# Optimization experiments

Hardware: AMD Instinct MI355X
Metric: run time of the kernel (lower is better)

Reference implementation:

```python
import jax, jax.numpy as jnp
import numpy as np

B, C_IN, C_OUT, H, W = 4, 256, 256, 64, 64
KH = KW = 3
STRIDE = 1
PAD = 1
DIL = 1


def setup_inputs() -> dict:
    key = jax.random.key(0)
    k1, k2, k3, k4 = jax.random.split(key, 4)
    x = jax.random.normal(k1, (B, C_IN, H, W), dtype=jnp.float32)
    # torchvision layout: 2*dg*KH*KW channels, (y, x) pair per kernel tap
    offset = jax.random.normal(k2, (B, 2 * KH * KW, H, W), dtype=jnp.float32)
    fan_in = C_IN * KH * KW
    weight = jax.random.normal(k3, (C_OUT, C_IN, KH, KW), dtype=jnp.float32) / np.sqrt(fan_in)
    bias = jax.random.normal(k4, (C_OUT,), dtype=jnp.float32) * 0.01
    return {"x": x, "offset": offset, "weight": weight, "bias": bias}


def _gather_bilinear_corner(x_flat, yi, xi, h, w):
    # x_flat: [B, C, H*W]; yi/xi: [B, KK, Ho, Wo] int32
    valid = ((yi >= 0) & (yi < h) & (xi >= 0) & (xi < w)).astype(x_flat.dtype)
    idx = jnp.clip(yi, 0, h - 1) * w + jnp.clip(xi, 0, w - 1)
    b = idx.shape[0]
    g = jnp.take_along_axis(x_flat, idx.reshape(b, 1, -1), axis=2)
    return g.reshape(b, x_flat.shape[1], *yi.shape[1:]), valid


def deform_conv2d(x, offset, weight, bias):
    b, c, h, w = x.shape
    o = weight.shape[0]
    kk = KH * KW
    ho = (h + 2 * PAD - DIL * (KH - 1) - 1) // STRIDE + 1
    wo = (w + 2 * PAD - DIL * (KW - 1) - 1) // STRIDE + 1

    ky = (jnp.arange(kk, dtype=jnp.float32) // KW) * DIL  # [KK]
    kx = (jnp.arange(kk, dtype=jnp.float32) % KW) * DIL
    hs = jnp.arange(ho, dtype=jnp.float32) * STRIDE - PAD   # [Ho]
    ws = jnp.arange(wo, dtype=jnp.float32) * STRIDE - PAD   # [Wo]

    off = offset.reshape(b, kk, 2, ho, wo)
    py = hs[None, None, :, None] + ky[None, :, None, None] + off[:, :, 0]  # [B,KK,Ho,Wo]
    px = ws[None, None, None, :] + kx[None, :, None, None] + off[:, :, 1]

    y0 = jnp.floor(py)
    x0 = jnp.floor(px)
    wy1 = py - y0  # fractional parts, differentiable w.r.t. offsets
    wx1 = px - x0
    wy0 = 1.0 - wy1
    wx0 = 1.0 - wx1
    y0i = y0.astype(jnp.int32)
    x0i = x0.astype(jnp.int32)

    x_flat = x.reshape(b, c, h * w)
    corners = [
        (y0i,     x0i,     wy0 * wx0),
        (y0i,     x0i + 1, wy0 * wx1),
        (y0i + 1, x0i,     wy1 * wx0),
        (y0i + 1, x0i + 1, wy1 * wx1),
    ]
    sampled = jnp.zeros((b, c, kk, ho, wo), dtype=x.dtype)
    for yi, xi, wgt in corners:
        g, valid = _gather_bilinear_corner(x_flat, yi, xi, h, w)
        sampled = sampled + g * (wgt * valid)[:, None]

    out = jnp.einsum('bckhw,ock->bohw', sampled, weight.reshape(o, c, kk))
    return out + bias[None, :, None, None]


def reference(x, offset, weight, bias):
    return deform_conv2d(x, offset, weight, bias)
```

## Files before the change

kernel.cpp:

```cpp
#include <hip/hip_runtime.h>

typedef __bf16 bf16;
typedef __bf16 bf16x4 __attribute__((ext_vector_type(4)));
typedef __bf16 bf16x8 __attribute__((ext_vector_type(8)));
typedef float  f32x4  __attribute__((ext_vector_type(4)));

#define CIN   256
#define KK    9
#define KDIM  2304
#define KITERS 72
#define PXW   64

__device__ __forceinline__ float sread(float f) {
    return __builtin_bit_cast(float,
        __builtin_amdgcn_readfirstlane(__builtin_bit_cast(int, f)));
}
__device__ __forceinline__ int sreadi(int v) {
    return __builtin_amdgcn_readfirstlane(v);
}

__global__ __launch_bounds__(256) void prep_k(const float* __restrict__ x,
                                              const float* __restrict__ w,
                                              bf16* __restrict__ xt,
                                              bf16* __restrict__ wq) {
    int bid = blockIdx.x;
    int tid = threadIdx.x;
    if (bid < 1024) {
        __shared__ bf16 tile[64][72];
        int pt = bid & 63, ct = (bid >> 6) & 3, b = bid >> 8;
        int lane = tid & 63, row = tid >> 6;
        const float* src = x + ((size_t)(b * 256 + ct * 64)) * 4096 + pt * 64;
        #pragma unroll
        for (int cc = row; cc < 64; cc += 4)
            tile[lane][cc] = (bf16)src[(size_t)cc * 4096 + lane];
        __syncthreads();
        bf16* dst = xt + ((size_t)(b * 4096 + pt * 64)) * 256 + ct * 64;
        int p = tid >> 3, j = tid & 7;
        #pragma unroll
        for (int pp = p; pp < 64; pp += 32)
            *reinterpret_cast<bf16x8*>(dst + (size_t)pp * 256 + j * 8) =
                *reinterpret_cast<const bf16x8*>(&tile[pp][j * 8]);
    } else {
        int idx  = (bid - 1024) * 256 + tid;
        int j    = idx & 7;
        int lane = (idx >> 3) & 63;
        int rest = idx >> 9;
        int kt   = rest % KITERS;
        int m    = rest / KITERS;
        int l16  = lane & 15;
        int quad = lane >> 4;
        int o    = m * 16 + l16;
        int k    = kt * 32 + quad * 8 + j;
        int tap  = k >> 8;
        int cc   = k & 255;
        wq[idx] = (bf16)w[(size_t)o * KDIM + cc * KK + tap];
    }
}

__global__ __launch_bounds__(1024, 4) void deform_gemm_k(
    const bf16*  __restrict__ xt,
    const float* __restrict__ off,
    const bf16*  __restrict__ wq,
    const float* __restrict__ bias,
    float*       __restrict__ out) {

    __shared__ bf16 S[PXW * 256];

    int tid   = threadIdx.x;
    int wavei = sreadi(tid >> 6);
    int lane  = tid & 63;
    int quad  = lane >> 4;
    int l16   = lane & 15;

    int bid   = blockIdx.x;
    int pb    = ((bid & 7) << 5) | (bid >> 3);
    int pix0  = pb * PXW;
    int b     = pix0 >> 12;
    int pimgb = pix0 & 4095;
    int obase = b * 73728;
    unsigned base = (unsigned)b * 1048576u + (unsigned)(lane * 4);

    f32x4 acc[4];
    #pragma unroll
    for (int nt = 0; nt < 4; ++nt)
        acc[nt] = (f32x4){0.f, 0.f, 0.f, 0.f};

    int q3 = lane & 7;

    for (int tap = 0; tap < KK; ++tap) {
        int ty = tap / 3 - 1;
        int tx = tap % 3 - 1;

        int u[4][4];
        float wt[4][4];
        #pragma unroll
        for (int i = 0; i < 4; ++i) {
            int pimg = pimgb + wavei * 4 + i;
            float oy = off[obase + pimg + (2 * tap) * 4096];
            float ox = off[obase + pimg + (2 * tap + 1) * 4096];
            float py = (float)((pimg >> 6) + ty) + oy;
            float px = (float)((pimg & 63) + tx) + ox;
            float fy = floorf(py), fx = floorf(px);
            int   y0 = (int)fy,    x0 = (int)fx;
            float wy1 = py - fy, wx1 = px - fx;
            float wy0 = 1.f - wy1, wx0 = 1.f - wx1;
            wy0 = ((unsigned)y0       < 64u) ? wy0 : 0.f;
            wy1 = ((unsigned)(y0 + 1) < 64u) ? wy1 : 0.f;
            wx0 = ((unsigned)x0       < 64u) ? wx0 : 0.f;
            wx1 = ((unsigned)(x0 + 1) < 64u) ? wx1 : 0.f;
            int yc0 = min(max(y0, 0), 63),     yc1 = min(max(y0 + 1, 0), 63);
            int xc0 = min(max(x0, 0), 63),     xc1 = min(max(x0 + 1, 0), 63);
            u[i][0] = sreadi((yc0 * 64 + xc0) * 256);
            u[i][1] = sreadi((yc0 * 64 + xc1) * 256);
            u[i][2] = sreadi((yc1 * 64 + xc0) * 256);
            u[i][3] = sreadi((yc1 * 64 + xc1) * 256);
            wt[i][0] = sread(wy0 * wx0); wt[i][1] = sread(wy0 * wx1);
            wt[i][2] = sread(wy1 * wx0); wt[i][3] = sread(wy1 * wx1);
        }
        bf16x4 v[4][4];
        #pragma unroll
        for (int i = 0; i < 4; ++i)
            #pragma unroll
            for (int j = 0; j < 4; ++j)
                v[i][j] = *reinterpret_cast<const bf16x4*>(xt + base + (unsigned)u[i][j]);
        #pragma unroll
        for (int i = 0; i < 4; ++i) {
            float a0 = 0.f, a1 = 0.f, a2 = 0.f, a3 = 0.f;
            #pragma unroll
            for (int j = 0; j < 4; ++j) {
                float wgt = wt[i][j];
                a0 += wgt * (float)v[i][j][0];
                a1 += wgt * (float)v[i][j][1];
                a2 += wgt * (float)v[i][j][2];
                a3 += wgt * (float)v[i][j][3];
            }
            bf16x4 sv;
            sv[0] = (bf16)a0; sv[1] = (bf16)a1;
            sv[2] = (bf16)a2; sv[3] = (bf16)a3;
            int n   = wavei * 4 + i;
            int gsw = (lane >> 1) ^ (n & 7);
            *reinterpret_cast<bf16x4*>(&S[n * 256 + gsw * 8 + (lane & 1) * 4]) = sv;
        }
        __syncthreads();

        const bf16* ap0 = wq + ((size_t)((wavei * KITERS + tap * 8) * 64 + lane)) * 8;
        #pragma unroll
        for (int kki = 0; kki < 8; ++kki) {
            bf16x8 a = *reinterpret_cast<const bf16x8*>(ap0 + (size_t)kki * 512);
            #pragma unroll
            for (int nt = 0; nt < 4; ++nt) {
                int row = nt * 16 + l16;
                int g   = (kki * 4 + quad) ^ q3;
                bf16x8 bb = *reinterpret_cast<const bf16x8*>(&S[row * 256 + g * 8]);
                acc[nt] = __builtin_amdgcn_mfma_f32_16x16x32_bf16(a, bb, acc[nt], 0, 0, 0);
            }
        }
        __syncthreads();
    }

    #pragma unroll
    for (int nt = 0; nt < 4; ++nt) {
        int pg   = pix0 + nt * 16 + l16;
        int bb_  = pg >> 12;
        int pimg = pg & 4095;
        int m    = wavei * 16 + quad * 4;
        float* op = out + ((size_t)(bb_ * 256 + m)) * 4096 + pimg;
        #pragma unroll
        for (int r = 0; r < 4; ++r)
            op[(size_t)r * 4096] = acc[nt][r] + bias[m + r];
    }
}

extern "C" void kernel_launch(void* const* d_in, const int* in_sizes, int n_in,
                              void* d_out, int out_size, void* d_ws, size_t ws_size,
                              hipStream_t stream) {
    const float* x    = (const float*)d_in[0];
    const float* off  = (const float*)d_in[1];
    const float* w    = (const float*)d_in[2];
    const float* bias = (const float*)d_in[3];
    float* out = (float*)d_out;

    bf16* wq = (bf16*)d_ws;
    bf16* xt = (bf16*)((char*)d_ws + (size_t)589824 * 2);

    prep_k<<<3328, 256, 0, stream>>>(x, w, xt, wq);
    deform_gemm_k<<<256, 1024, 0, stream>>>(xt, off, wq, bias, out);
}
```

Baseline: 121.2 us.

## Warp-specialize deform conv into gather producers and MFMA consumers with slot ring

Splits the 16 waves into 8 producer waves that do the bilinear gather into a 3-slot LDS ring of half-tap chunks and 8 consumer waves that run the MFMAs. Each consumer wave now computes two output-row tiles. Producers and consumers coordinate through shared-memory ready/freed counters with spin-sleep instead of block-wide barriers. The aim is to overlap gather latency with matrix math. The cost is that only half the waves gather and half compute, consumers carry doubled accumulators, and busy-wait polling is added.

```diff
diff --git a/kernel.cpp b/kernel.cpp
--- a/kernel.cpp
+++ b/kernel.cpp
@@ -10,6 +10,8 @@
 #define KDIM  2304
 #define KITERS 72
 #define PXW   64
+#define NSLOT 3
+#define SLOT_ELEMS (PXW * 128)
 
 __device__ __forceinline__ float sread(float f) {
     return __builtin_bit_cast(float,
@@ -57,14 +59,16 @@
     }
 }
 
-__global__ __launch_bounds__(1024, 4) void deform_gemm_k(
+__global__ __launch_bounds__(1024) void deform_gemm_k(
     const bf16*  __restrict__ xt,
     const float* __restrict__ off,
     const bf16*  __restrict__ wq,
     const float* __restrict__ bias,
     float*       __restrict__ out) {
 
-    __shared__ bf16 S[PXW * 256];
+    __shared__ bf16 S[NSLOT * SLOT_ELEMS];
+    __shared__ int ready[NSLOT];
+    __shared__ int freed[NSLOT];
 
     int tid   = threadIdx.x;
     int wavei = sreadi(tid >> 6);
@@ -78,96 +82,133 @@
     int b     = pix0 >> 12;
     int pimgb = pix0 & 4095;
     int obase = b * 73728;
-    unsigned base = (unsigned)b * 1048576u + (unsigned)(lane * 4);
-
-    f32x4 acc[4];
-    #pragma unroll
-    for (int nt = 0; nt < 4; ++nt)
-        acc[nt] = (f32x4){0.f, 0.f, 0.f, 0.f};
-
-    int q3 = lane & 7;
-
-    for (int tap = 0; tap < KK; ++tap) {
-        int ty = tap / 3 - 1;
-        int tx = tap % 3 - 1;
-
-        int u[4][4];
-        float wt[4][4];
-        #pragma unroll
-        for (int i = 0; i < 4; ++i) {
-            int pimg = pimgb + wavei * 4 + i;
-            float oy = off[obase + pimg + (2 * tap) * 4096];
-            float ox = off[obase + pimg + (2 * tap + 1) * 4096];
-            float py = (float)((pimg >> 6) + ty) + oy;
-            float px = (float)((pimg & 63) + tx) + ox;
-            float fy = floorf(py), fx = floorf(px);
-            int   y0 = (int)fy,    x0 = (int)fx;
-            float wy1 = py - fy, wx1 = px - fx;
-            float wy0 = 1.f - wy1, wx0 = 1.f - wx1;
-            wy0 = ((unsigned)y0       < 64u) ? wy0 : 0.f;
-            wy1 = ((unsigned)(y0 + 1) < 64u) ? wy1 : 0.f;
-            wx0 = ((unsigned)x0       < 64u) ? wx0 : 0.f;
-            wx1 = ((unsigned)(x0 + 1) < 64u) ? wx1 : 0.f;
-            int yc0 = min(max(y0, 0), 63),     yc1 = min(max(y0 + 1, 0), 63);
-            int xc0 = min(max(x0, 0), 63),     xc1 = min(max(x0 + 1, 0), 63);
-            u[i][0] = sreadi((yc0 * 64 + xc0) * 256);
-            u[i][1] = sreadi((yc0 * 64 + xc1) * 256);
-            u[i][2] = sreadi((yc1 * 64 + xc0) * 256);
-            u[i][3] = sreadi((yc1 * 64 + xc1) * 256);
-            wt[i][0] = sread(wy0 * wx0); wt[i][1] = sread(wy0 * wx1);
-            wt[i][2] = sread(wy1 * wx0); wt[i][3] = sread(wy1 * wx1);
+
+    if (tid < NSLOT) { ready[tid] = 0; freed[tid] = 0; }
+    __syncthreads();
+
+    if (wavei < 8) {
+        int pw = wavei;
+        unsigned base = (unsigned)b * 1048576u + (unsigned)(lane * 4);
+        for (int tap = 0; tap < KK; ++tap) {
+            int ty = tap / 3 - 1;
+            int tx = tap % 3 - 1;
+            int h0 = 2 * tap,     s0 = h0 % 3, g0 = h0 / 3;
+            int h1 = 2 * tap + 1, s1 = h1 % 3, g1 = h1 / 3;
+            while (*(volatile int*)&freed[s0] < 8 * g0) __builtin_amdgcn_s_sleep(2);
+            while (*(volatile int*)&freed[s1] < 8 * g1) __builtin_amdgcn_s_sleep(2);
+
+            #pragma unroll
+            for (int gq = 0; gq < 2; ++gq) {
+                int u[4][4];
+                float wt[4][4];
+                #pragma unroll
+                for (int i = 0; i < 4; ++i) {
+                    int n    = pw * 8 + gq * 4 + i;
+                    int pimg = pimgb + n;
+                    float oy = off[obase + pimg + (2 * tap) * 4096];
+                    float ox = off[obase + pimg + (2 * tap + 1) * 4096];
+                    float py = (float)((pimg >> 6) + ty) + oy;
+                    float px = (float)((pimg & 63) + tx) + ox;
+                    float fy = floorf(py), fx = floorf(px);
+                    int   y0 = (int)fy,    x0 = (int)fx;
+                    float wy1 = py - fy, wx1 = px - fx;
+                    float wy0 = 1.f - wy1, wx0 = 1.f - wx1;
+                    wy0 = ((unsigned)y0       < 64u) ? wy0 : 0.f;
+                    wy1 = ((unsigned)(y0 + 1) < 64u) ? wy1 : 0.f;
+                    wx0 = ((unsigned)x0       < 64u) ? wx0 : 0.f;
+                    wx1 = ((unsigned)(x0 + 1) < 64u) ? wx1 : 0.f;
+                    int yc0 = min(max(y0, 0), 63), yc1 = min(max(y0 + 1, 0), 63);
+                    int xc0 = min(max(x0, 0), 63), xc1 = min(max(x0 + 1, 0), 63);
+                    u[i][0] = sreadi((yc0 * 64 + xc0) * 256);
+                    u[i][1] = sreadi((yc0 * 64 + xc1) * 256);
+                    u[i][2] = sreadi((yc1 * 64 + xc0) * 256);
+                    u[i][3] = sreadi((yc1 * 64 + xc1) * 256);
+                    wt[i][0] = sread(wy0 * wx0); wt[i][1] = sread(wy0 * wx1);
+                    wt[i][2] = sread(wy1 * wx0); wt[i][3] = sread(wy1 * wx1);
+                }
+                bf16x4 v[4][4];
+                #pragma unroll
+                for (int i = 0; i < 4; ++i)
+                    #pragma unroll
+                    for (int j = 0; j < 4; ++j)
+                        v[i][j] = *reinterpret_cast<const bf16x4*>(
+                            xt + base + (unsigned)u[i][j]);
+                #pragma unroll
+                for (int i = 0; i < 4; ++i) {
+                    float a0 = 0.f, a1 = 0.f, a2 = 0.f, a3 = 0.f;
+                    #pragma unroll
+                    for (int j = 0; j < 4; ++j) {
+                        float wgt = wt[i][j];
+                        a0 += wgt * (float)v[i][j][0];
+                        a1 += wgt * (float)v[i][j][1];
+                        a2 += wgt * (float)v[i][j][2];
+                        a3 += wgt * (float)v[i][j][3];
+                    }
+                    bf16x4 sv;
+                    sv[0] = (bf16)a0; sv[1] = (bf16)a1;
+                    sv[2] = (bf16)a2; sv[3] = (bf16)a3;
+                    int n    = pw * 8 + gq * 4 + i;
+                    int slot = (lane >= 32) ? s1 : s0;
+                    int gw   = (lane & 31) >> 1;
+                    int gs   = (gw & 8) | ((gw ^ (n & 7)) & 7);
+                    *reinterpret_cast<bf16x4*>(
+                        &S[slot * SLOT_ELEMS + n * 128 + gs * 8 + (lane & 1) * 4]) = sv;
+                }
+            }
+            __threadfence_block();
+            if (lane == 0) { atomicAdd(&ready[s0], 1); atomicAdd(&ready[s1], 1); }
         }
-        bf16x4 v[4][4];
-        #pragma unroll
-        for (int i = 0; i < 4; ++i)
-            #pragma unroll
-            for (int j = 0; j < 4; ++j)
-                v[i][j] = *reinterpret_cast<const bf16x4*>(xt + base + (unsigned)u[i][j]);
-        #pragma unroll
-        for (int i = 0; i < 4; ++i) {
-            float a0 = 0.f, a1 = 0.f, a2 = 0.f, a3 = 0.f;
-            #pragma unroll
-            for (int j = 0; j < 4; ++j) {
-                float wgt = wt[i][j];
-                a0 += wgt * (float)v[i][j][0];
-                a1 += wgt * (float)v[i][j][1];
-                a2 += wgt * (float)v[i][j][2];
-                a3 += wgt * (float)v[i][j][3];
+    } else {
+        int cw = wavei - 8;
+        f32x4 acc[2][4];
+        #pragma unroll
+        for (int mt = 0; mt < 2; ++mt)
+            #pragma unroll
+            for (int nt = 0; nt < 4; ++nt)
+                acc[mt][nt] = (f32x4){0.f, 0.f, 0.f, 0.f};
+
+        for (int h = 0; h < 2 * KK; ++h) {
+            int s = h % 3, g = h / 3;
+            int tap = h >> 1, kh = h & 1;
+            while (*(volatile int*)&ready[s] < 8 * (g + 1)) __builtin_amdgcn_s_sleep(2);
+            __threadfence_block();
+            const bf16* sb = &S[s * SLOT_ELEMS];
+            #pragma unroll
+            for (int kki = 0; kki < 4; ++kki) {
+                int kt = tap * 8 + kh * 4 + kki;
+                const bf16* ap = wq +
+                    ((size_t)(((2 * cw) * KITERS + kt) * 64 + lane)) * 8;
+                bf16x8 a0 = *reinterpret_cast<const bf16x8*>(ap);
+                bf16x8 a1 = *reinterpret_cast<const bf16x8*>(ap + (size_t)KITERS * 64 * 8);
+                int gidx = kki * 4 + quad;
+                #pragma unroll
+                for (int nt = 0; nt < 4; ++nt) {
+                    int row = nt * 16 + l16;
+                    int gs  = (gidx & 8) | ((gidx ^ (row & 7)) & 7);
+                    bf16x8 bb = *reinterpret_cast<const bf16x8*>(
+                        sb + row * 128 + gs * 8);
+                    acc[0][nt] = __builtin_amdgcn_mfma_f32_16x16x32_bf16(a0, bb, acc[0][nt], 0, 0, 0);
+                    acc[1][nt] = __builtin_amdgcn_mfma_f32_16x16x32_bf16(a1, bb, acc[1][nt], 0, 0, 0);
+                }
             }
-            bf16x4 sv;
-            sv[0] = (bf16)a0; sv[1] = (bf16)a1;
-            sv[2] = (bf16)a2; sv[3] = (bf16)a3;
-            int n   = wavei * 4 + i;
-            int gsw = (lane >> 1) ^ (n & 7);
-            *reinterpret_cast<bf16x4*>(&S[n * 256 + gsw * 8 + (lane & 1) * 4]) = sv;
+            __threadfence_block();
+            if (lane == 0) atomicAdd(&freed[s], 1);
         }
-        __syncthreads();
-
-        const bf16* ap0 = wq + ((size_t)((wavei * KITERS + tap * 8) * 64 + lane)) * 8;
-        #pragma unroll
-        for (int kki = 0; kki < 8; ++kki) {
-            bf16x8 a = *reinterpret_cast<const bf16x8*>(ap0 + (size_t)kki * 512);
-            #pragma unroll
-            for (int nt = 0; nt < 4; ++nt) {
-                int row = nt * 16 + l16;
-                int g   = (kki * 4 + quad) ^ q3;
-                bf16x8 bb = *reinterpret_cast<const bf16x8*>(&S[row * 256 + g * 8]);
-                acc[nt] = __builtin_amdgcn_mfma_f32_16x16x32_bf16(a, bb, acc[nt], 0, 0, 0);
+
+        #pragma unroll
+        for (int nt = 0; nt < 4; ++nt) {
+            int pg   = pix0 + nt * 16 + l16;
+            int bb_  = pg >> 12;
+            int pimg = pg & 4095;
+            #pragma unroll
+            for (int mt = 0; mt < 2; ++mt) {
+                int m = (2 * cw + mt) * 16 + quad * 4;
+                float* op = out + ((size_t)(bb_ * 256 + m)) * 4096 + pimg;
+                #pragma unroll
+                for (int r = 0; r < 4; ++r)
+                    op[(size_t)r * 4096] = acc[mt][nt][r] + bias[m + r];
             }
         }
-        __syncthreads();
-    }
-
-    #pragma unroll
-    for (int nt = 0; nt < 4; ++nt) {
-        int pg   = pix0 + nt * 16 + l16;
-        int bb_  = pg >> 12;
-        int pimg = pg & 4095;
-        int m    = wavei * 16 + quad * 4;
-        float* op = out + ((size_t)(bb_ * 256 + m)) * 4096 + pimg;
-        #pragma unroll
-        for (int r = 0; r < 4; ++r)
-            op[(size_t)r * 4096] = acc[nt][r] + bias[m + r];
     }
 }
 
```

After: 126.1 us. 1.04x slower.

## Halve pixel tile, double-buffer LDS, stagger tap order across blocks

Applied to the files above, without the earlier changes.

Cuts the pixels per block from 64 to 32 and doubles the grid to 512 blocks, so there are more blocks than CUs and the work is spread more evenly. The shared sample buffer is double-buffered, which removes the second barrier in each tap iteration. Neighbouring blocks start at different taps (rotated by 4) so they read different weight slices at the same time. The trade-off is that each weight tile loaded from global memory now feeds half as many MFMAs, which doubles total weight traffic.

```diff
diff --git a/kernel.cpp b/kernel.cpp
--- a/kernel.cpp
+++ b/kernel.cpp
@@ -9,7 +9,7 @@
 #define KK    9
 #define KDIM  2304
 #define KITERS 72
-#define PXW   64
+#define PXW   32
 
 __device__ __forceinline__ float sread(float f) {
     return __builtin_bit_cast(float,
@@ -57,14 +57,14 @@
     }
 }
 
-__global__ __launch_bounds__(1024, 4) void deform_gemm_k(
+__global__ __launch_bounds__(1024, 8) void deform_gemm_k(
     const bf16*  __restrict__ xt,
     const float* __restrict__ off,
     const bf16*  __restrict__ wq,
     const float* __restrict__ bias,
     float*       __restrict__ out) {
 
-    __shared__ bf16 S[PXW * 256];
+    __shared__ bf16 S[2][PXW * 256];
 
     int tid   = threadIdx.x;
     int wavei = sreadi(tid >> 6);
@@ -73,29 +73,28 @@
     int l16   = lane & 15;
 
     int bid   = blockIdx.x;
-    int pb    = ((bid & 7) << 5) | (bid >> 3);
+    int pb    = ((bid & 7) << 6) | (bid >> 3);
     int pix0  = pb * PXW;
     int b     = pix0 >> 12;
     int pimgb = pix0 & 4095;
     int obase = b * 73728;
     unsigned base = (unsigned)b * 1048576u + (unsigned)(lane * 4);
+    int rot   = ((bid >> 3) & 1) * 4;
 
-    f32x4 acc[4];
-    #pragma unroll
-    for (int nt = 0; nt < 4; ++nt)
-        acc[nt] = (f32x4){0.f, 0.f, 0.f, 0.f};
+    f32x4 acc[2];
+    acc[0] = (f32x4){0.f, 0.f, 0.f, 0.f};
+    acc[1] = (f32x4){0.f, 0.f, 0.f, 0.f};
 
-    int q3 = lane & 7;
-
-    for (int tap = 0; tap < KK; ++tap) {
+    for (int t = 0; t < KK; ++t) {
+        int tap = t + rot; if (tap >= KK) tap -= KK;
         int ty = tap / 3 - 1;
         int tx = tap % 3 - 1;
+        bf16* Sw = &S[t & 1][0];
 
-        int u[4][4];
-        float wt[4][4];
         #pragma unroll
-        for (int i = 0; i < 4; ++i) {
-            int pimg = pimgb + wavei * 4 + i;
+        for (int i = 0; i < 2; ++i) {
+            int n    = wavei * 2 + i;
+            int pimg = pimgb + n;
             float oy = off[obase + pimg + (2 * tap) * 4096];
             float ox = off[obase + pimg + (2 * tap + 1) * 4096];
             float py = (float)((pimg >> 6) + ty) + oy;
@@ -108,63 +107,56 @@
             wy1 = ((unsigned)(y0 + 1) < 64u) ? wy1 : 0.f;
             wx0 = ((unsigned)x0       < 64u) ? wx0 : 0.f;
             wx1 = ((unsigned)(x0 + 1) < 64u) ? wx1 : 0.f;
-            int yc0 = min(max(y0, 0), 63),     yc1 = min(max(y0 + 1, 0), 63);
-            int xc0 = min(max(x0, 0), 63),     xc1 = min(max(x0 + 1, 0), 63);
-            u[i][0] = sreadi((yc0 * 64 + xc0) * 256);
-            u[i][1] = sreadi((yc0 * 64 + xc1) * 256);
-            u[i][2] = sreadi((yc1 * 64 + xc0) * 256);
-            u[i][3] = sreadi((yc1 * 64 + xc1) * 256);
-            wt[i][0] = sread(wy0 * wx0); wt[i][1] = sread(wy0 * wx1);
-            wt[i][2] = sread(wy1 * wx0); wt[i][3] = sread(wy1 * wx1);
-        }
-        bf16x4 v[4][4];
-        #pragma unroll
-        for (int i = 0; i < 4; ++i)
-            #pragma unroll
-            for (int j = 0; j < 4; ++j)
-                v[i][j] = *reinterpret_cast<const bf16x4*>(xt + base + (unsigned)u[i][j]);
-        #pragma unroll
-        for (int i = 0; i < 4; ++i) {
-            float a0 = 0.f, a1 = 0.f, a2 = 0.f, a3 = 0.f;
-            #pragma unroll
-            for (int j = 0; j < 4; ++j) {
-                float wgt = wt[i][j];
-                a0 += wgt * (float)v[i][j][0];
-                a1 += wgt * (float)v[i][j][1];
-                a2 += wgt * (float)v[i][j][2];
-                a3 += wgt * (float)v[i][j][3];
-            }
+            int yc0 = min(max(y0, 0), 63), yc1 = min(max(y0 + 1, 0), 63);
+            int xc0 = min(max(x0, 0), 63), xc1 = min(max(x0 + 1, 0), 63);
+            int u0 = sreadi((yc0 * 64 + xc0) * 256);
+            int u1 = sreadi((yc0 * 64 + xc1) * 256);
+            int u2 = sreadi((yc1 * 64 + xc0) * 256);
+            int u3 = sreadi((yc1 * 64 + xc1) * 256);
+            float w0 = sread(wy0 * wx0), w1 = sread(wy0 * wx1);
+            float w2 = sread(wy1 * wx0), w3 = sread(wy1 * wx1);
+            bf16x4 v0 = *reinterpret_cast<const bf16x4*>(xt + base + (unsigned)u0);
+            bf16x4 v1 = *reinterpret_cast<const bf16x4*>(xt + base + (unsigned)u1);
+            bf16x4 v2 = *reinterpret_cast<const bf16x4*>(xt + base + (unsigned)u2);
+            bf16x4 v3 = *reinterpret_cast<const bf16x4*>(xt + base + (unsigned)u3);
+            float a0 = w0 * (float)v0[0] + w1 * (float)v1[0]
+                     + w2 * (float)v2[0] + w3 * (float)v3[0];
+            float a1 = w0 * (float)v0[1] + w1 * (float)v1[1]
+                     + w2 * (float)v2[1] + w3 * (float)v3[1];
+            float a2 = w0 * (float)v0[2] + w1 * (float)v1[2]
+                     + w2 * (float)v2[2] + w3 * (float)v3[2];
+            float a3 = w0 * (float)v0[3] + w1 * (float)v1[3]
+                     + w2 * (float)v2[3] + w3 * (float)v3[3];
             bf16x4 sv;
             sv[0] = (bf16)a0; sv[1] = (bf16)a1;
             sv[2] = (bf16)a2; sv[3] = (bf16)a3;
-            int n   = wavei * 4 + i;
-            int gsw = (lane >> 1) ^ (n & 7);
-            *reinterpret_cast<bf16x4*>(&S[n * 256 + gsw * 8 + (lane & 1) * 4]) = sv;
+            int gw = lane >> 1;
+            int gs = (gw & 24) | ((gw ^ (n & 7)) & 7);
+            *reinterpret_cast<bf16x4*>(Sw + n * 256 + gs * 8 + (lane & 1) * 4) = sv;
         }
         __syncthreads();
 
+        const bf16* Sr  = Sw;
         const bf16* ap0 = wq + ((size_t)((wavei * KITERS + tap * 8) * 64 + lane)) * 8;
         #pragma unroll
         for (int kki = 0; kki < 8; ++kki) {
             bf16x8 a = *reinterpret_cast<const bf16x8*>(ap0 + (size_t)kki * 512);
-            #pragma unroll
-            for (int nt = 0; nt < 4; ++nt) {
-                int row = nt * 16 + l16;
-                int g   = (kki * 4 + quad) ^ q3;
-                bf16x8 bb = *reinterpret_cast<const bf16x8*>(&S[row * 256 + g * 8]);
-                acc[nt] = __builtin_amdgcn_mfma_f32_16x16x32_bf16(a, bb, acc[nt], 0, 0, 0);
-            }
+            int g  = kki * 4 + quad;
+            int gs = (g & 24) | ((g ^ (l16 & 7)) & 7);
+            bf16x8 b0 = *reinterpret_cast<const bf16x8*>(Sr + l16 * 256 + gs * 8);
+            bf16x8 b1 = *reinterpret_cast<const bf16x8*>(Sr + (16 + l16) * 256 + gs * 8);
+            acc[0] = __builtin_amdgcn_mfma_f32_16x16x32_bf16(a, b0, acc[0], 0, 0, 0);
+            acc[1] = __builtin_amdgcn_mfma_f32_16x16x32_bf16(a, b1, acc[1], 0, 0, 0);
         }
-        __syncthreads();
     }
 
     #pragma unroll
-    for (int nt = 0; nt < 4; ++nt) {
+    for (int nt = 0; nt < 2; ++nt) {
         int pg   = pix0 + nt * 16 + l16;
-        int bb_  = pg >> 12;
+        int bb   = pg >> 12;
         int pimg = pg & 4095;
         int m    = wavei * 16 + quad * 4;
-        float* op = out + ((size_t)(bb_ * 256 + m)) * 4096 + pimg;
+        float* op = out + ((size_t)(bb * 256 + m)) * 4096 + pimg;
         #pragma unroll
         for (int r = 0; r < 4; ++r)
             op[(size_t)r * 4096] = acc[nt][r] + bias[m + r];
@@ -184,5 +176,5 @@
     bf16* xt = (bf16*)((char*)d_ws + (size_t)589824 * 2);
 
     prep_k<<<3328, 256, 0, stream>>>(x, w, xt, wq);
-    deform_gemm_k<<<256, 1024, 0, stream>>>(xt, off, wq, bias, out);
+    deform_gemm_k<<<512, 1024, 0, stream>>>(xt, off, wq, bias, out);
 }
```

After: 117.2 us. 3.3% less time.
